# Performance work log

Hardware: AMD Instinct MI355X
Metric: run time of the kernel (lower is better)

Reference implementation:

```python
import jax, jax.numpy as jnp
import numpy as np

N = 8192
IN_F = 512
OUT_F = 128
NEG_BIG = -9.0e15


def setup_inputs() -> dict:
    key = jax.random.key(0)
    k_x, k_adj, k_w, k_a1, k_a2 = jax.random.split(key, 5)
    X = jax.random.normal(k_x, (N, IN_F), dtype=jnp.float32)
    adj = jax.random.randint(k_adj, (N, N), 0, 2, dtype=jnp.int32)
    # xavier_uniform with gain=1.414
    gain = 1.414
    lim_w = gain * np.sqrt(6.0 / (IN_F + OUT_F))
    W = jax.random.uniform(k_w, (IN_F, OUT_F), minval=-lim_w, maxval=lim_w, dtype=jnp.float32)
    lim_a = gain * np.sqrt(6.0 / (OUT_F + 1))
    a_1 = jax.random.uniform(k_a1, (OUT_F, 1), minval=-lim_a, maxval=lim_a, dtype=jnp.float32)
    a_2 = jax.random.uniform(k_a2, (OUT_F, 1), minval=-lim_a, maxval=lim_a, dtype=jnp.float32)
    return {"X": X, "adj": adj, "W": W, "a_1": a_1, "a_2": a_2}


def reference(X, adj, W, a_1, a_2):
    h = X @ W                         # [N, out]
    Wh1 = h @ a_1                     # [N, 1]
    Wh2 = h @ a_2                     # [N, 1]
    alpha = Wh1 + Wh2.T               # [N, N] broadcast score sum
    s = jax.nn.sigmoid(alpha)
    masked = jnp.where(adj > 0, s, jnp.float32(NEG_BIG))
    attn = jax.nn.softmax(masked, axis=1)  # dropout p=0.0 -> identity
    return attn @ h                   # [N, out]
```

## Files before the change

### kernel.cpp

```cpp
#include <hip/hip_runtime.h>
#include <hip/hip_bf16.h>

#define N_NODES 8192
#define IN_F 512
#define OUT_F 128
#define NSTRIPE 8
#define KT_PER 32
#define NWORDS (N_NODES / 32)
#define LOG2E 1.4426950408889634f

typedef unsigned short u16;
typedef unsigned int u32;
typedef short s16x8 __attribute__((ext_vector_type(8)));
typedef float f32x4 __attribute__((ext_vector_type(4)));
typedef u32 u32x4 __attribute__((ext_vector_type(4)));

__device__ __forceinline__ u16 f2bf(float f) {
    union { float f; unsigned u; } x; x.f = f;
    unsigned r = x.u + 0x7FFFu + ((x.u >> 16) & 1u);
    return (u16)(r >> 16);
}

__device__ __forceinline__ u32 packbf2(float a, float b) {
    __hip_bfloat162 h = __float22bfloat162_rn(make_float2(a, b));
    u32 u; __builtin_memcpy(&u, &h, 4);
    return u;
}

__device__ __forceinline__ float edge_p(float wh1, float w2, int keep) {
    float alpha = wh1 + w2;
    float e = exp2f(-LOG2E * alpha);
    float s = __builtin_amdgcn_rcpf(1.0f + e);
    float p = exp2f(LOG2E * s);
    return keep ? p : 0.0f;
}

__global__ void repack_W(const float* __restrict__ W, u16* __restrict__ W_frag) {
    int tid = blockIdx.x * 256 + threadIdx.x;
    int j = tid & 7;
    int lane = (tid >> 3) & 63;
    int nt = (tid >> 9) & 7;
    int kt = tid >> 12;
    int k = kt * 32 + (lane >> 4) * 8 + j;
    int n = nt * 16 + (lane & 15);
    W_frag[tid] = f2bf(W[k * OUT_F + n]);
}

__global__ void compute_Wa(const float* __restrict__ W, const float* __restrict__ a1,
                           const float* __restrict__ a2,
                           float* __restrict__ Wa1, float* __restrict__ Wa2) {
    int k = blockIdx.x * 256 + threadIdx.x;
    if (k >= IN_F) return;
    float s1 = 0.f, s2 = 0.f;
    #pragma unroll 8
    for (int n = 0; n < OUT_F; n++) {
        float w = W[k * OUT_F + n];
        s1 += w * a1[n];
        s2 += w * a2[n];
    }
    Wa1[k] = s1; Wa2[k] = s2;
}

__global__ __launch_bounds__(256)
void pack_adj(const int* __restrict__ adj, u32* __restrict__ Pk) {
    int gid = blockIdx.x * 256 + threadIdx.x;
    const int* src = adj + (size_t)gid * 32;
    u32 b = 0;
    #pragma unroll
    for (int t = 0; t < 8; t++) {
        int4 v = *(const int4*)(src + t * 4);
        b |= (u32)(v.x > 0) << (t * 4 + 0);
        b |= (u32)(v.y > 0) << (t * 4 + 1);
        b |= (u32)(v.z > 0) << (t * 4 + 2);
        b |= (u32)(v.w > 0) << (t * 4 + 3);
    }
    Pk[gid] = b;
}

__global__ __launch_bounds__(256)
void gemm_h(const float* __restrict__ X, const u16* __restrict__ W_frag,
            const float* __restrict__ Wa1, const float* __restrict__ Wa2,
            float* __restrict__ Wh1, float* __restrict__ Wh2,
            u16* __restrict__ h_frag) {
    int tid = threadIdx.x;
    int wave = tid >> 6;
    int lane = tid & 63;
    int quad = lane >> 4;
    int lid = lane & 15;
    int rbase = blockIdx.x * 16;
    const float* xrow = X + (size_t)(rbase + lid) * IN_F;
    const s16x8* Wf = (const s16x8*)W_frag;
    f32x4 acc0 = {}, acc1 = {};
    float p1 = 0.f, p2 = 0.f;
    int nt0 = wave * 2;

    for (int kt = 0; kt < 16; kt++) {
        int k0 = kt * 32 + quad * 8;
        float4 x0 = *(const float4*)(xrow + k0);
        float4 x1 = *(const float4*)(xrow + k0 + 4);
        u32x4 uv;
        uv.x = packbf2(x0.x, x0.y); uv.y = packbf2(x0.z, x0.w);
        uv.z = packbf2(x1.x, x1.y); uv.w = packbf2(x1.z, x1.w);
        s16x8 a = __builtin_bit_cast(s16x8, uv);
        if (wave == 0) {
            float4 wa = *(const float4*)(Wa1 + k0);
            float4 wb = *(const float4*)(Wa1 + k0 + 4);
            float4 wc = *(const float4*)(Wa2 + k0);
            float4 wd = *(const float4*)(Wa2 + k0 + 4);
            p1 += x0.x*wa.x + x0.y*wa.y + x0.z*wa.z + x0.w*wa.w
                + x1.x*wb.x + x1.y*wb.y + x1.z*wb.z + x1.w*wb.w;
            p2 += x0.x*wc.x + x0.y*wc.y + x0.z*wc.z + x0.w*wc.w
                + x1.x*wd.x + x1.y*wd.y + x1.z*wd.z + x1.w*wd.w;
        }
        s16x8 b0 = Wf[(kt * 8 + nt0) * 64 + lane];
        s16x8 b1 = Wf[(kt * 8 + nt0 + 1) * 64 + lane];
        acc0 = __builtin_amdgcn_mfma_f32_16x16x32_bf16(a, b0, acc0, 0, 0, 0);
        acc1 = __builtin_amdgcn_mfma_f32_16x16x32_bf16(a, b1, acc1, 0, 0, 0);
    }

    #pragma unroll
    for (int reg = 0; reg < 4; reg++) {
        int row = rbase + quad * 4 + reg;
        int ktile = row >> 5, kl = row & 31;
        int lane2 = (kl >> 3) * 16 + lid, j2 = kl & 7;
        h_frag[(size_t)((ktile * 8 + nt0) * 64 + lane2) * 8 + j2] = f2bf(acc0[reg]);
        h_frag[(size_t)((ktile * 8 + nt0 + 1) * 64 + lane2) * 8 + j2] = f2bf(acc1[reg]);
    }
    if (wave == 0) {
        p1 += __shfl_xor(p1, 16, 64); p1 += __shfl_xor(p1, 32, 64);
        p2 += __shfl_xor(p2, 16, 64); p2 += __shfl_xor(p2, 32, 64);
        if (lane < 16) { Wh1[rbase + lid] = p1; Wh2[rbase + lid] = p2; }
    }
}

__global__ __launch_bounds__(512)
void attn_fused(const u32* __restrict__ Pk, const float* __restrict__ Wh1,
                const float* __restrict__ Wh2, const u16* __restrict__ h_frag,
                float* __restrict__ out) {
    __shared__ f32x4 red[NSTRIPE][16][64];
    __shared__ float rsum_lds[NSTRIPE][32];

    int tid = threadIdx.x;
    int wave = tid >> 6;
    int lane = tid & 63;
    int quad = lane >> 4;
    int lid = lane & 15;
    int rbase = blockIdx.x * 32;
    int r0 = rbase + lid, r1 = r0 + 16;

    float wh10 = Wh1[r0], wh11 = Wh1[r1];
    f32x4 acc0[8] = {}, acc1[8] = {};
    float ps0 = 0.f, ps1 = 0.f;
    const s16x8* Hf = (const s16x8*)h_frag;
    const u32* prow0 = Pk + (size_t)r0 * NWORDS;
    const u32* prow1 = Pk + (size_t)r1 * NWORDS;

    const int kt0 = wave * KT_PER;

    u32x4 P0 = *(const u32x4*)(prow0 + kt0);
    u32x4 P1 = *(const u32x4*)(prow1 + kt0);

    #pragma unroll 1
    for (int g = 0; g < KT_PER / 4; g++) {
        u32x4 c0 = P0, c1 = P1;
        int gn = (g + 1 < KT_PER / 4) ? g + 1 : g;
        P0 = *(const u32x4*)(prow0 + kt0 + gn * 4);
        P1 = *(const u32x4*)(prow1 + kt0 + gn * 4);

        #pragma unroll
        for (int t = 0; t < 4; t++) {
            int kt = kt0 + g * 4 + t;
            int k0 = kt * 32 + quad * 8;
            u32 w0 = c0[t] >> (quad * 8);
            u32 w1 = c1[t] >> (quad * 8);
            float4 w20 = *(const float4*)(Wh2 + k0);
            float4 w21 = *(const float4*)(Wh2 + k0 + 4);

            float e0 = edge_p(wh10, w20.x, (w0 >> 0) & 1);
            float e1 = edge_p(wh10, w20.y, (w0 >> 1) & 1);
            float e2 = edge_p(wh10, w20.z, (w0 >> 2) & 1);
            float e3 = edge_p(wh10, w20.w, (w0 >> 3) & 1);
            float e4 = edge_p(wh10, w21.x, (w0 >> 4) & 1);
            float e5 = edge_p(wh10, w21.y, (w0 >> 5) & 1);
            float e6 = edge_p(wh10, w21.z, (w0 >> 6) & 1);
            float e7 = edge_p(wh10, w21.w, (w0 >> 7) & 1);
            ps0 += ((e0 + e1) + (e2 + e3)) + ((e4 + e5) + (e6 + e7));
            u32x4 uv0;
            uv0.x = packbf2(e0, e1); uv0.y = packbf2(e2, e3);
            uv0.z = packbf2(e4, e5); uv0.w = packbf2(e6, e7);

            float f0 = edge_p(wh11, w20.x, (w1 >> 0) & 1);
            float f1 = edge_p(wh11, w20.y, (w1 >> 1) & 1);
            float f2 = edge_p(wh11, w20.z, (w1 >> 2) & 1);
            float f3 = edge_p(wh11, w20.w, (w1 >> 3) & 1);
            float f4 = edge_p(wh11, w21.x, (w1 >> 4) & 1);
            float f5 = edge_p(wh11, w21.y, (w1 >> 5) & 1);
            float f6 = edge_p(wh11, w21.z, (w1 >> 6) & 1);
            float f7 = edge_p(wh11, w21.w, (w1 >> 7) & 1);
            ps1 += ((f0 + f1) + (f2 + f3)) + ((f4 + f5) + (f6 + f7));
            u32x4 uv1;
            uv1.x = packbf2(f0, f1); uv1.y = packbf2(f2, f3);
            uv1.z = packbf2(f4, f5); uv1.w = packbf2(f6, f7);

            s16x8 af0 = __builtin_bit_cast(s16x8, uv0);
            s16x8 af1 = __builtin_bit_cast(s16x8, uv1);

            #pragma unroll
            for (int nt = 0; nt < 8; nt++) {
                s16x8 b = Hf[(kt * 8 + nt) * 64 + lane];
                acc0[nt] = __builtin_amdgcn_mfma_f32_16x16x32_bf16(af0, b, acc0[nt], 0, 0, 0);
                acc1[nt] = __builtin_amdgcn_mfma_f32_16x16x32_bf16(af1, b, acc1[nt], 0, 0, 0);
            }
        }
    }

    ps0 += __shfl_xor(ps0, 16, 64); ps0 += __shfl_xor(ps0, 32, 64);
    ps1 += __shfl_xor(ps1, 16, 64); ps1 += __shfl_xor(ps1, 32, 64);
    if (lane < 16) {
        rsum_lds[wave][lane] = ps0;
        rsum_lds[wave][lane + 16] = ps1;
    }

    #pragma unroll
    for (int nt = 0; nt < 8; nt++) {
        red[wave][nt][lane] = acc0[nt];
        red[wave][nt + 8][lane] = acc1[nt];
    }
    __syncthreads();

    #pragma unroll
    for (int half = 0; half < 2; half++) {
        int i = wave + half * 8;
        int rowoff = half * 16;
        f32x4 s = red[0][i][lane];
        #pragma unroll
        for (int p2 = 1; p2 < NSTRIPE; p2++) s += red[p2][i][lane];

        #pragma unroll
        for (int reg = 0; reg < 4; reg++) {
            int rowl = quad * 4 + reg;
            float sum = 0.f;
            #pragma unroll
            for (int p2 = 0; p2 < NSTRIPE; p2++) sum += rsum_lds[p2][rowoff + rowl];
            float r = __builtin_amdgcn_rcpf(sum);
            r = r * (2.0f - sum * r);
            out[(size_t)(rbase + rowoff + rowl) * OUT_F + wave * 16 + lid] = s[reg] * r;
        }
    }
}

extern "C" void kernel_launch(void* const* d_in, const int* in_sizes, int n_in,
                              void* d_out, int out_size, void* d_ws, size_t ws_size,
                              hipStream_t stream) {
    const float* X   = (const float*)d_in[0];
    const int*   adj = (const int*)d_in[1];
    const float* W   = (const float*)d_in[2];
    const float* a1  = (const float*)d_in[3];
    const float* a2  = (const float*)d_in[4];

    char* ws = (char*)d_ws;
    float* Wh1 = (float*)(ws);
    float* Wh2 = (float*)(ws + (32 << 10));
    float* Wa1 = (float*)(ws + (64 << 10));
    float* Wa2 = (float*)(ws + (66 << 10));
    u16* W_frag = (u16*)(ws + (128 << 10));
    u16* h_frag = (u16*)(ws + (256 << 10));
    u32* Pk     = (u32*)(ws + ((size_t)4 << 20));
    float* out = (float*)d_out;

    hipLaunchKernelGGL(repack_W, dim3(256), dim3(256), 0, stream, W, W_frag);
    hipLaunchKernelGGL(compute_Wa, dim3(2), dim3(256), 0, stream, W, a1, a2, Wa1, Wa2);
    hipLaunchKernelGGL(pack_adj, dim3(N_NODES * NWORDS / 256), dim3(256), 0, stream, adj, Pk);
    hipLaunchKernelGGL(gemm_h, dim3(512), dim3(256), 0, stream,
                       X, W_frag, Wa1, Wa2, Wh1, Wh2, h_frag);
    hipLaunchKernelGGL(attn_fused, dim3(N_NODES / 32), dim3(512), 0, stream,
                       Pk, Wh1, Wh2, h_frag, out);
}
```

Before: 469.2 us.

## Software-pipeline loads in gemm and attention kernels, stage Wh2 in LDS

In gemm_h the X, W fragment and attention-vector loads for the next k-tile are issued before computing the current one. In attn_fused the Wh2 vector is copied into LDS (aliasing the reduction buffer) once per block, and the h fragments for the next k-tile are double-buffered in registers so global loads overlap the MFMAs. The aim is to hide global memory latency in the inner loops. In exchange it costs extra registers (16 s16x8 buffers), which may reduce occupancy, and adds barriers around the LDS reuse.

```diff
diff --git a/kernel.cpp b/kernel.cpp
--- a/kernel.cpp
+++ b/kernel.cpp
@@ -94,26 +94,43 @@
     float p1 = 0.f, p2 = 0.f;
     int nt0 = wave * 2;
 
+    int k0p = quad * 8;
+    float4 X0 = *(const float4*)(xrow + k0p);
+    float4 X1 = *(const float4*)(xrow + k0p + 4);
+    s16x8 B0 = Wf[nt0 * 64 + lane];
+    s16x8 B1 = Wf[(nt0 + 1) * 64 + lane];
+    float4 A0 = {}, A1 = {}, C0 = {}, C1 = {};
+    if (wave == 0) {
+        A0 = *(const float4*)(Wa1 + k0p); A1 = *(const float4*)(Wa1 + k0p + 4);
+        C0 = *(const float4*)(Wa2 + k0p); C1 = *(const float4*)(Wa2 + k0p + 4);
+    }
+
+    #pragma unroll 1
     for (int kt = 0; kt < 16; kt++) {
-        int k0 = kt * 32 + quad * 8;
-        float4 x0 = *(const float4*)(xrow + k0);
-        float4 x1 = *(const float4*)(xrow + k0 + 4);
+        float4 x0 = X0, x1 = X1;
+        s16x8 b0 = B0, b1 = B1;
+        float4 wa = A0, wb = A1, wc = C0, wd = C1;
+        int ktn = (kt + 1 < 16) ? kt + 1 : kt;
+        int k0n = ktn * 32 + quad * 8;
+        X0 = *(const float4*)(xrow + k0n);
+        X1 = *(const float4*)(xrow + k0n + 4);
+        B0 = Wf[(ktn * 8 + nt0) * 64 + lane];
+        B1 = Wf[(ktn * 8 + nt0 + 1) * 64 + lane];
+        if (wave == 0) {
+            A0 = *(const float4*)(Wa1 + k0n); A1 = *(const float4*)(Wa1 + k0n + 4);
+            C0 = *(const float4*)(Wa2 + k0n); C1 = *(const float4*)(Wa2 + k0n + 4);
+        }
+
         u32x4 uv;
         uv.x = packbf2(x0.x, x0.y); uv.y = packbf2(x0.z, x0.w);
         uv.z = packbf2(x1.x, x1.y); uv.w = packbf2(x1.z, x1.w);
         s16x8 a = __builtin_bit_cast(s16x8, uv);
         if (wave == 0) {
-            float4 wa = *(const float4*)(Wa1 + k0);
-            float4 wb = *(const float4*)(Wa1 + k0 + 4);
-            float4 wc = *(const float4*)(Wa2 + k0);
-            float4 wd = *(const float4*)(Wa2 + k0 + 4);
             p1 += x0.x*wa.x + x0.y*wa.y + x0.z*wa.z + x0.w*wa.w
                 + x1.x*wb.x + x1.y*wb.y + x1.z*wb.z + x1.w*wb.w;
             p2 += x0.x*wc.x + x0.y*wc.y + x0.z*wc.z + x0.w*wc.w
                 + x1.x*wd.x + x1.y*wd.y + x1.z*wd.z + x1.w*wd.w;
         }
-        s16x8 b0 = Wf[(kt * 8 + nt0) * 64 + lane];
-        s16x8 b1 = Wf[(kt * 8 + nt0 + 1) * 64 + lane];
         acc0 = __builtin_amdgcn_mfma_f32_16x16x32_bf16(a, b0, acc0, 0, 0, 0);
         acc1 = __builtin_amdgcn_mfma_f32_16x16x32_bf16(a, b1, acc1, 0, 0, 0);
     }
@@ -139,6 +156,7 @@
                 float* __restrict__ out) {
     __shared__ f32x4 red[NSTRIPE][16][64];
     __shared__ float rsum_lds[NSTRIPE][32];
+    float* Wh2_lds = (float*)&red[0][0][0];
 
     int tid = threadIdx.x;
     int wave = tid >> 6;
@@ -148,70 +166,87 @@
     int rbase = blockIdx.x * 32;
     int r0 = rbase + lid, r1 = r0 + 16;
 
+    {
+        const float4* s = (const float4*)Wh2;
+        float4* d = (float4*)Wh2_lds;
+        #pragma unroll
+        for (int i = 0; i < 4; i++) d[tid + i * 512] = s[tid + i * 512];
+    }
     float wh10 = Wh1[r0], wh11 = Wh1[r1];
+    __syncthreads();
+
     f32x4 acc0[8] = {}, acc1[8] = {};
     float ps0 = 0.f, ps1 = 0.f;
     const s16x8* Hf = (const s16x8*)h_frag;
     const u32* prow0 = Pk + (size_t)r0 * NWORDS;
     const u32* prow1 = Pk + (size_t)r1 * NWORDS;
-
     const int kt0 = wave * KT_PER;
 
-    u32x4 P0 = *(const u32x4*)(prow0 + kt0);
-    u32x4 P1 = *(const u32x4*)(prow1 + kt0);
+    u32x4 PA = *(const u32x4*)(prow0 + kt0);
+    u32x4 PB = *(const u32x4*)(prow1 + kt0);
+    s16x8 hb0[8], hb1[8];
+    #pragma unroll
+    for (int nt = 0; nt < 8; nt++) hb0[nt] = Hf[(kt0 * 8 + nt) * 64 + lane];
+
+    auto step = [&](int i, u32 pw0, u32 pw1, s16x8 (&cur)[8], s16x8 (&nxt)[8]) {
+        int kt = kt0 + i;
+        int ktn = (i + 1 < KT_PER) ? kt + 1 : kt;
+        #pragma unroll
+        for (int nt = 0; nt < 8; nt++) nxt[nt] = Hf[(ktn * 8 + nt) * 64 + lane];
+
+        int k0 = kt * 32 + quad * 8;
+        float4 w20 = *(const float4*)(Wh2_lds + k0);
+        float4 w21 = *(const float4*)(Wh2_lds + k0 + 4);
+        u32 w0 = pw0 >> (quad * 8);
+        u32 w1 = pw1 >> (quad * 8);
+
+        float e0 = edge_p(wh10, w20.x, (w0 >> 0) & 1);
+        float e1 = edge_p(wh10, w20.y, (w0 >> 1) & 1);
+        float e2 = edge_p(wh10, w20.z, (w0 >> 2) & 1);
+        float e3 = edge_p(wh10, w20.w, (w0 >> 3) & 1);
+        float e4 = edge_p(wh10, w21.x, (w0 >> 4) & 1);
+        float e5 = edge_p(wh10, w21.y, (w0 >> 5) & 1);
+        float e6 = edge_p(wh10, w21.z, (w0 >> 6) & 1);
+        float e7 = edge_p(wh10, w21.w, (w0 >> 7) & 1);
+        ps0 += ((e0 + e1) + (e2 + e3)) + ((e4 + e5) + (e6 + e7));
+        u32x4 uv0;
+        uv0.x = packbf2(e0, e1); uv0.y = packbf2(e2, e3);
+        uv0.z = packbf2(e4, e5); uv0.w = packbf2(e6, e7);
+
+        float f0 = edge_p(wh11, w20.x, (w1 >> 0) & 1);
+        float f1 = edge_p(wh11, w20.y, (w1 >> 1) & 1);
+        float f2 = edge_p(wh11, w20.z, (w1 >> 2) & 1);
+        float f3 = edge_p(wh11, w20.w, (w1 >> 3) & 1);
+        float f4 = edge_p(wh11, w21.x, (w1 >> 4) & 1);
+        float f5 = edge_p(wh11, w21.y, (w1 >> 5) & 1);
+        float f6 = edge_p(wh11, w21.z, (w1 >> 6) & 1);
+        float f7 = edge_p(wh11, w21.w, (w1 >> 7) & 1);
+        ps1 += ((f0 + f1) + (f2 + f3)) + ((f4 + f5) + (f6 + f7));
+        u32x4 uv1;
+        uv1.x = packbf2(f0, f1); uv1.y = packbf2(f2, f3);
+        uv1.z = packbf2(f4, f5); uv1.w = packbf2(f6, f7);
+
+        s16x8 af0 = __builtin_bit_cast(s16x8, uv0);
+        s16x8 af1 = __builtin_bit_cast(s16x8, uv1);
+
+        #pragma unroll
+        for (int nt = 0; nt < 8; nt++) {
+            acc0[nt] = __builtin_amdgcn_mfma_f32_16x16x32_bf16(af0, cur[nt], acc0[nt], 0, 0, 0);
+            acc1[nt] = __builtin_amdgcn_mfma_f32_16x16x32_bf16(af1, cur[nt], acc1[nt], 0, 0, 0);
+        }
+    };
 
     #pragma unroll 1
     for (int g = 0; g < KT_PER / 4; g++) {
-        u32x4 c0 = P0, c1 = P1;
-        int gn = (g + 1 < KT_PER / 4) ? g + 1 : g;
-        P0 = *(const u32x4*)(prow0 + kt0 + gn * 4);
-        P1 = *(const u32x4*)(prow1 + kt0 + gn * 4);
-
-        #pragma unroll
-        for (int t = 0; t < 4; t++) {
-            int kt = kt0 + g * 4 + t;
-            int k0 = kt * 32 + quad * 8;
-            u32 w0 = c0[t] >> (quad * 8);
-            u32 w1 = c1[t] >> (quad * 8);
-            float4 w20 = *(const float4*)(Wh2 + k0);
-            float4 w21 = *(const float4*)(Wh2 + k0 + 4);
-
-            float e0 = edge_p(wh10, w20.x, (w0 >> 0) & 1);
-            float e1 = edge_p(wh10, w20.y, (w0 >> 1) & 1);
-            float e2 = edge_p(wh10, w20.z, (w0 >> 2) & 1);
-            float e3 = edge_p(wh10, w20.w, (w0 >> 3) & 1);
-            float e4 = edge_p(wh10, w21.x, (w0 >> 4) & 1);
-            float e5 = edge_p(wh10, w21.y, (w0 >> 5) & 1);
-            float e6 = edge_p(wh10, w21.z, (w0 >> 6) & 1);
-            float e7 = edge_p(wh10, w21.w, (w0 >> 7) & 1);
-            ps0 += ((e0 + e1) + (e2 + e3)) + ((e4 + e5) + (e6 + e7));
-            u32x4 uv0;
-            uv0.x = packbf2(e0, e1); uv0.y = packbf2(e2, e3);
-            uv0.z = packbf2(e4, e5); uv0.w = packbf2(e6, e7);
-
-            float f0 = edge_p(wh11, w20.x, (w1 >> 0) & 1);
-            float f1 = edge_p(wh11, w20.y, (w1 >> 1) & 1);
-            float f2 = edge_p(wh11, w20.z, (w1 >> 2) & 1);
-            float f3 = edge_p(wh11, w20.w, (w1 >> 3) & 1);
-            float f4 = edge_p(wh11, w21.x, (w1 >> 4) & 1);
-            float f5 = edge_p(wh11, w21.y, (w1 >> 5) & 1);
-            float f6 = edge_p(wh11, w21.z, (w1 >> 6) & 1);
-            float f7 = edge_p(wh11, w21.w, (w1 >> 7) & 1);
-            ps1 += ((f0 + f1) + (f2 + f3)) + ((f4 + f5) + (f6 + f7));
-            u32x4 uv1;
-            uv1.x = packbf2(f0, f1); uv1.y = packbf2(f2, f3);
-            uv1.z = packbf2(f4, f5); uv1.w = packbf2(f6, f7);
-
-            s16x8 af0 = __builtin_bit_cast(s16x8, uv0);
-            s16x8 af1 = __builtin_bit_cast(s16x8, uv1);
-
-            #pragma unroll
-            for (int nt = 0; nt < 8; nt++) {
-                s16x8 b = Hf[(kt * 8 + nt) * 64 + lane];
-                acc0[nt] = __builtin_amdgcn_mfma_f32_16x16x32_bf16(af0, b, acc0[nt], 0, 0, 0);
-                acc1[nt] = __builtin_amdgcn_mfma_f32_16x16x32_bf16(af1, b, acc1[nt], 0, 0, 0);
-            }
-        }
+        int base = g * 4;
+        u32x4 cPA = PA, cPB = PB;
+        int gb = (g + 1 < KT_PER / 4) ? (kt0 + base + 4) : kt0;
+        PA = *(const u32x4*)(prow0 + gb);
+        PB = *(const u32x4*)(prow1 + gb);
+        step(base + 0, cPA.x, cPB.x, hb0, hb1);
+        step(base + 1, cPA.y, cPB.y, hb1, hb0);
+        step(base + 2, cPA.z, cPB.z, hb0, hb1);
+        step(base + 3, cPA.w, cPB.w, hb1, hb0);
     }
 
     ps0 += __shfl_xor(ps0, 16, 64); ps0 += __shfl_xor(ps0, 32, 64);
@@ -220,6 +255,8 @@
         rsum_lds[wave][lane] = ps0;
         rsum_lds[wave][lane + 16] = ps1;
     }
+
+    __syncthreads();
 
     #pragma unroll
     for (int nt = 0; nt < 8; nt++) {
```

After: 452.3 us. 3.6% less time.
